# Performance work log

Hardware: AMD Instinct MI355X
Metric: run time of the kernel (lower is better)

The kernel has to match this reference:

```python
import jax, jax.numpy as jnp
from jax import lax
import numpy as np

B, T, D = 8192, 187, 1
H, C = 128, 5


def setup_inputs() -> dict:
    key = jax.random.key(0)
    k1, k2, k3, k4 = jax.random.split(key, 4)
    x = jax.random.normal(k1, (B, T, D), dtype=jnp.float32)
    # SimpleRNN params: kernel W [D,H], recurrent kernel U [H,H] (orthogonal-ish), bias b [H]
    W = jax.random.normal(k2, (D, H), dtype=jnp.float32) * (1.0 / np.sqrt(D))
    U = jax.random.normal(k3, (H, H), dtype=jnp.float32) * (1.0 / np.sqrt(H))
    b = jnp.zeros((H,), dtype=jnp.float32)
    # Dense head params
    Wd = jax.random.normal(k4, (H, C), dtype=jnp.float32) * (1.0 / np.sqrt(H))
    bd = jnp.zeros((C,), dtype=jnp.float32)
    return {"x": x, "W": W, "U": U, "b": b, "Wd": Wd, "bd": bd}


def reference(x, W, U, b, Wd, bd):
    # SimpleRNN (tanh) recurrence over time, returning final hidden state only
    # (return_sequences=False, dropout inactive at inference).
    h0 = jnp.zeros((x.shape[0], U.shape[0]), dtype=x.dtype)
    xt_seq = jnp.swapaxes(x, 0, 1)  # [T, B, D]

    def step(h, xt):
        h_new = jnp.tanh(xt @ W + h @ U + b)
        return h_new, None

    hT, _ = lax.scan(step, h0, xt_seq)
    # Dense softmax classifier head
    logits = hT @ Wd + bd  # [B, C]
    return jax.nn.softmax(logits, axis=-1)
```

## Files before the change

### kernel.cpp

```cpp
#include <hip/hip_runtime.h>
#include <hip/hip_bf16.h>


#define BT 8192
#define TS 187
#define HD 128
#define NC 5

typedef float    f32x4  __attribute__((ext_vector_type(4)));
typedef _Float16 f16x8  __attribute__((ext_vector_type(8)));
typedef __fp16   fp16x2 __attribute__((ext_vector_type(2)));
typedef unsigned int u32;
typedef u32      u32x2  __attribute__((ext_vector_type(2)));

__device__ __forceinline__ float tanh_fast(float v) {
    float e = __expf(2.0f * v);
    float r = __builtin_amdgcn_rcpf(e + 1.0f);
    return fmaf(-2.0f, r, 1.0f);
}

__device__ __forceinline__ u32 pk16(float a, float b) {
    fp16x2 p = __builtin_amdgcn_cvt_pkrtz(a, b);
    return __builtin_bit_cast(u32, p);
}

union frag_u { f16x8 v; u32 w[4]; };

__device__ __forceinline__ void pin_frag(f16x8& f) {
    frag_u pu; pu.v = f;
    asm volatile("" : "+v"(pu.w[0]), "+v"(pu.w[1]), "+v"(pu.w[2]), "+v"(pu.w[3]));
    f = pu.v;
}

__global__ __launch_bounds__(512, 4)
void rnn_fused(const float* __restrict__ xg, const float* __restrict__ wg,
               const float* __restrict__ ug, const float* __restrict__ bg,
               const float* __restrict__ wdg, const float* __restrict__ bdg,
               float* __restrict__ outg)
{
    __shared__ u32   xb[2][4][64][4];
    __shared__ float xs[TS][16];
    __shared__ float lg[8][16][NC];

    const int tid  = threadIdx.x;
    const int w    = tid >> 6;
    const int lane = tid & 63;
    const int l15  = lane & 15;
    const int l4   = lane >> 4;
    const int b0   = blockIdx.x * 16;
    const int Tw   = w >> 1;
    const int hw   = w & 1;

    #pragma unroll
    for (int r = 0; r < 6; ++r) {
        const int idx = r * 512 + tid;
        const int bb  = idx / 192;
        const int ss  = idx % 192;
        if (ss < TS)
            xs[ss][bb] = xg[(long)(b0 + bb) * TS + ss];
    }

    f16x8 uf0, uf1, uf2, uf3;
    {
        const int j = 16*w + l15;
        #pragma unroll
        for (int e = 0; e < 8; ++e) {
            const int i = 16*(e>>2) + 4*l4 + (e&3);
            uf0[e] = (_Float16)ug[(i      )*HD + j];
            uf1[e] = (_Float16)ug[(i + 32 )*HD + j];
            uf2[e] = (_Float16)ug[(i + 64 )*HD + j];
            uf3[e] = (_Float16)ug[(i + 96 )*HD + j];
        }
    }
    pin_frag(uf0); pin_frag(uf1); pin_frag(uf2); pin_frag(uf3);

    float wv[4], bv[4];
    #pragma unroll
    for (int q = 0; q < 4; ++q) {
        const int j = 16*w + 4*l4 + q;
        wv[q] = wg[j];
        bv[q] = bg[j];
    }

    f16x8 h0 = (f16x8)(_Float16)0.0f;
    f16x8 h1 = h0, h2 = h0, h3 = h0;

    __syncthreads();
    float xv = xs[0][l15];

    f32x4 acc;

#define STEP(BUF, SN)                                                       \
    {                                                                       \
        const float xnext = xs[(SN)][l15];                                  \
        f32x4 a0, a1;                                                       \
        _Pragma("unroll") for (int q = 0; q < 4; ++q) {                     \
            a0[q] = fmaf(xv, wv[q], bv[q]); a1[q] = 0.0f;                   \
        }                                                                   \
        a0 = __builtin_amdgcn_mfma_f32_16x16x32_f16(uf0, h0, a0, 0, 0, 0);  \
        a1 = __builtin_amdgcn_mfma_f32_16x16x32_f16(uf2, h2, a1, 0, 0, 0);  \
        a0 = __builtin_amdgcn_mfma_f32_16x16x32_f16(uf1, h1, a0, 0, 0, 0);  \
        a1 = __builtin_amdgcn_mfma_f32_16x16x32_f16(uf3, h3, a1, 0, 0, 0);  \
        _Pragma("unroll") for (int q = 0; q < 4; ++q)                       \
            acc[q] = tanh_fast(a0[q] + a1[q]);                              \
        u32x2 pk;                                                           \
        pk[0] = pk16(acc[0], acc[1]);                                       \
        pk[1] = pk16(acc[2], acc[3]);                                       \
        *(u32x2*)&xb[(BUF)][Tw][lane][2*hw] = pk;                           \
        __syncthreads();                                                    \
        h0 = *(const f16x8*)&xb[(BUF)][0][lane][0];                         \
        h1 = *(const f16x8*)&xb[(BUF)][1][lane][0];                         \
        h2 = *(const f16x8*)&xb[(BUF)][2][lane][0];                         \
        h3 = *(const f16x8*)&xb[(BUF)][3][lane][0];                         \
        xv = xnext;                                                         \
    }

    for (int k = 0; k < 93; ++k) {
        STEP(0, 2*k + 1);
        STEP(1, 2*k + 2);
    }
    STEP(0, TS - 1);
#undef STEP

    float p[NC];
    #pragma unroll
    for (int c = 0; c < NC; ++c) p[c] = 0.0f;
    #pragma unroll
    for (int q = 0; q < 4; ++q) {
        const int j = 16*w + 4*l4 + q;
        #pragma unroll
        for (int c = 0; c < NC; ++c)
            p[c] = fmaf(acc[q], wdg[j*NC + c], p[c]);
    }
    #pragma unroll
    for (int c = 0; c < NC; ++c) {
        p[c] += __shfl_xor(p[c], 16, 64);
        p[c] += __shfl_xor(p[c], 32, 64);
    }
    if (l4 == 0) {
        #pragma unroll
        for (int c = 0; c < NC; ++c) lg[w][l15][c] = p[c];
    }
    __syncthreads();

    if (tid < 16) {
        float l[NC];
        #pragma unroll
        for (int c = 0; c < NC; ++c) {
            l[c] = bdg[c];
            #pragma unroll
            for (int ww = 0; ww < 8; ++ww) l[c] += lg[ww][tid][c];
        }
        float m = l[0];
        #pragma unroll
        for (int c = 1; c < NC; ++c) m = fmaxf(m, l[c]);
        float e[NC], ssum = 0.0f;
        #pragma unroll
        for (int c = 0; c < NC; ++c) { e[c] = __expf(l[c] - m); ssum += e[c]; }
        const float rs = 1.0f / ssum;
        #pragma unroll
        for (int c = 0; c < NC; ++c)
            outg[(long)(b0 + tid)*NC + c] = e[c] * rs;
    }
}

extern "C" void kernel_launch(void* const* d_in, const int* in_sizes, int n_in,
                              void* d_out, int out_size, void* d_ws, size_t ws_size,
                              hipStream_t stream) {
    const float* x  = (const float*)d_in[0];
    const float* W  = (const float*)d_in[1];
    const float* U  = (const float*)d_in[2];
    const float* b  = (const float*)d_in[3];
    const float* Wd = (const float*)d_in[4];
    const float* bd = (const float*)d_in[5];
    float* out = (float*)d_out;

    rnn_fused<<<BT / 16, 512, 0, stream>>>(x, W, U, b, Wd, bd, out);
}
```

Before: 85.42 us.

## Process two batch tiles per block and fold tanh scaling into weights

Each block now handles 32 batch rows as two independent 16-row tiles. Their MFMA chains and tanh computations interleave, so the latency of one tile's dependent recurrence can be hidden behind the other's, and there is one barrier per step for both tiles. The 2*log2(e) factor is folded into U, W and b at load time, so tanh uses a raw exp2 and the bias enters as the MFMA accumulator init. The trade-off is half as many blocks (256), more registers and LDS per block, and a lowered occupancy hint, which may leave CUs underused on a 256-CU part.

```diff
diff --git a/kernel.cpp b/kernel.cpp
--- a/kernel.cpp
+++ b/kernel.cpp
@@ -13,8 +13,18 @@
 typedef unsigned int u32;
 typedef u32      u32x2  __attribute__((ext_vector_type(2)));
 
-__device__ __forceinline__ float tanh_fast(float v) {
-    float e = __expf(2.0f * v);
+#define PRE 2.885390081777927f
+
+__device__ __forceinline__ float exp2_fast(float v) {
+#if __has_builtin(__builtin_amdgcn_exp2f)
+    return __builtin_amdgcn_exp2f(v);
+#else
+    return exp2f(v);
+#endif
+}
+
+__device__ __forceinline__ float tanh_pre(float vp) {
+    float e = exp2_fast(vp);
     float r = __builtin_amdgcn_rcpf(e + 1.0f);
     return fmaf(-2.0f, r, 1.0f);
 }
@@ -32,32 +42,34 @@
     f = pu.v;
 }
 
-__global__ __launch_bounds__(512, 4)
+__global__ __launch_bounds__(512, 2)
 void rnn_fused(const float* __restrict__ xg, const float* __restrict__ wg,
                const float* __restrict__ ug, const float* __restrict__ bg,
                const float* __restrict__ wdg, const float* __restrict__ bdg,
                float* __restrict__ outg)
 {
-    __shared__ u32   xb[2][4][64][4];
-    __shared__ float xs[TS][16];
-    __shared__ float lg[8][16][NC];
+    __shared__ u32   xbA[2][4][64][4];
+    __shared__ u32   xbB[2][4][64][4];
+    __shared__ float xs2[2][TS][16];
+    __shared__ float lgA[8][16][NC];
+    __shared__ float lgB[8][16][NC];
 
     const int tid  = threadIdx.x;
     const int w    = tid >> 6;
     const int lane = tid & 63;
     const int l15  = lane & 15;
     const int l4   = lane >> 4;
-    const int b0   = blockIdx.x * 16;
+    const int b0   = blockIdx.x * 32;
     const int Tw   = w >> 1;
     const int hw   = w & 1;
 
     #pragma unroll
-    for (int r = 0; r < 6; ++r) {
+    for (int r = 0; r < 12; ++r) {
         const int idx = r * 512 + tid;
         const int bb  = idx / 192;
         const int ss  = idx % 192;
         if (ss < TS)
-            xs[ss][bb] = xg[(long)(b0 + bb) * TS + ss];
+            xs2[bb >> 4][ss][bb & 15] = xg[(long)(b0 + bb) * TS + ss];
     }
 
     f16x8 uf0, uf1, uf2, uf3;
@@ -66,53 +78,67 @@
         #pragma unroll
         for (int e = 0; e < 8; ++e) {
             const int i = 16*(e>>2) + 4*l4 + (e&3);
-            uf0[e] = (_Float16)ug[(i      )*HD + j];
-            uf1[e] = (_Float16)ug[(i + 32 )*HD + j];
-            uf2[e] = (_Float16)ug[(i + 64 )*HD + j];
-            uf3[e] = (_Float16)ug[(i + 96 )*HD + j];
+            uf0[e] = (_Float16)(PRE * ug[(i      )*HD + j]);
+            uf1[e] = (_Float16)(PRE * ug[(i + 32 )*HD + j]);
+            uf2[e] = (_Float16)(PRE * ug[(i + 64 )*HD + j]);
+            uf3[e] = (_Float16)(PRE * ug[(i + 96 )*HD + j]);
         }
     }
     pin_frag(uf0); pin_frag(uf1); pin_frag(uf2); pin_frag(uf3);
 
-    float wv[4], bv[4];
+    float wv[4]; f32x4 bvv;
     #pragma unroll
     for (int q = 0; q < 4; ++q) {
         const int j = 16*w + 4*l4 + q;
-        wv[q] = wg[j];
-        bv[q] = bg[j];
-    }
-
-    f16x8 h0 = (f16x8)(_Float16)0.0f;
-    f16x8 h1 = h0, h2 = h0, h3 = h0;
+        wv[q]  = PRE * wg[j];
+        bvv[q] = PRE * bg[j];
+    }
+
+    f16x8 hA0 = (f16x8)(_Float16)0.0f;
+    f16x8 hA1 = hA0, hA2 = hA0, hA3 = hA0;
+    f16x8 hB0 = hA0, hB1 = hA0, hB2 = hA0, hB3 = hA0;
 
     __syncthreads();
-    float xv = xs[0][l15];
-
-    f32x4 acc;
-
-#define STEP(BUF, SN)                                                       \
-    {                                                                       \
-        const float xnext = xs[(SN)][l15];                                  \
-        f32x4 a0, a1;                                                       \
-        _Pragma("unroll") for (int q = 0; q < 4; ++q) {                     \
-            a0[q] = fmaf(xv, wv[q], bv[q]); a1[q] = 0.0f;                   \
-        }                                                                   \
-        a0 = __builtin_amdgcn_mfma_f32_16x16x32_f16(uf0, h0, a0, 0, 0, 0);  \
-        a1 = __builtin_amdgcn_mfma_f32_16x16x32_f16(uf2, h2, a1, 0, 0, 0);  \
-        a0 = __builtin_amdgcn_mfma_f32_16x16x32_f16(uf1, h1, a0, 0, 0, 0);  \
-        a1 = __builtin_amdgcn_mfma_f32_16x16x32_f16(uf3, h3, a1, 0, 0, 0);  \
-        _Pragma("unroll") for (int q = 0; q < 4; ++q)                       \
-            acc[q] = tanh_fast(a0[q] + a1[q]);                              \
-        u32x2 pk;                                                           \
-        pk[0] = pk16(acc[0], acc[1]);                                       \
-        pk[1] = pk16(acc[2], acc[3]);                                       \
-        *(u32x2*)&xb[(BUF)][Tw][lane][2*hw] = pk;                           \
-        __syncthreads();                                                    \
-        h0 = *(const f16x8*)&xb[(BUF)][0][lane][0];                         \
-        h1 = *(const f16x8*)&xb[(BUF)][1][lane][0];                         \
-        h2 = *(const f16x8*)&xb[(BUF)][2][lane][0];                         \
-        h3 = *(const f16x8*)&xb[(BUF)][3][lane][0];                         \
-        xv = xnext;                                                         \
+    float xvA = xs2[0][0][l15];
+    float xvB = xs2[1][0][l15];
+
+    f32x4 accA, accB;
+
+#define STEP(BUF, SN)                                                        \
+    {                                                                        \
+        const float xAn = xs2[0][(SN)][l15];                                 \
+        const float xBn = xs2[1][(SN)][l15];                                 \
+        f32x4 a0, a1, c0, c1;                                                \
+        _Pragma("unroll") for (int q = 0; q < 4; ++q) {                      \
+            a0[q] = xvA * wv[q]; c0[q] = xvB * wv[q];                        \
+        }                                                                    \
+        a0 = __builtin_amdgcn_mfma_f32_16x16x32_f16(uf0, hA0, a0,  0, 0, 0); \
+        c0 = __builtin_amdgcn_mfma_f32_16x16x32_f16(uf0, hB0, c0,  0, 0, 0); \
+        a1 = __builtin_amdgcn_mfma_f32_16x16x32_f16(uf2, hA2, bvv, 0, 0, 0); \
+        c1 = __builtin_amdgcn_mfma_f32_16x16x32_f16(uf2, hB2, bvv, 0, 0, 0); \
+        a0 = __builtin_amdgcn_mfma_f32_16x16x32_f16(uf1, hA1, a0,  0, 0, 0); \
+        c0 = __builtin_amdgcn_mfma_f32_16x16x32_f16(uf1, hB1, c0,  0, 0, 0); \
+        a1 = __builtin_amdgcn_mfma_f32_16x16x32_f16(uf3, hA3, a1,  0, 0, 0); \
+        c1 = __builtin_amdgcn_mfma_f32_16x16x32_f16(uf3, hB3, c1,  0, 0, 0); \
+        _Pragma("unroll") for (int q = 0; q < 4; ++q) {                      \
+            accA[q] = tanh_pre(a0[q] + a1[q]);                               \
+            accB[q] = tanh_pre(c0[q] + c1[q]);                               \
+        }                                                                    \
+        u32x2 pA, pB;                                                        \
+        pA[0] = pk16(accA[0], accA[1]); pA[1] = pk16(accA[2], accA[3]);      \
+        pB[0] = pk16(accB[0], accB[1]); pB[1] = pk16(accB[2], accB[3]);      \
+        *(u32x2*)&xbA[(BUF)][Tw][lane][2*hw] = pA;                           \
+        *(u32x2*)&xbB[(BUF)][Tw][lane][2*hw] = pB;                           \
+        __syncthreads();                                                     \
+        hA0 = *(const f16x8*)&xbA[(BUF)][0][lane][0];                        \
+        hA1 = *(const f16x8*)&xbA[(BUF)][1][lane][0];                        \
+        hA2 = *(const f16x8*)&xbA[(BUF)][2][lane][0];                        \
+        hA3 = *(const f16x8*)&xbA[(BUF)][3][lane][0];                        \
+        hB0 = *(const f16x8*)&xbB[(BUF)][0][lane][0];                        \
+        hB1 = *(const f16x8*)&xbB[(BUF)][1][lane][0];                        \
+        hB2 = *(const f16x8*)&xbB[(BUF)][2][lane][0];                        \
+        hB3 = *(const f16x8*)&xbB[(BUF)][3][lane][0];                        \
+        xvA = xAn; xvB = xBn;                                                \
     }
 
     for (int k = 0; k < 93; ++k) {
@@ -122,34 +148,41 @@
     STEP(0, TS - 1);
 #undef STEP
 
-    float p[NC];
-    #pragma unroll
-    for (int c = 0; c < NC; ++c) p[c] = 0.0f;
+    float pA[NC], pB[NC];
+    #pragma unroll
+    for (int c = 0; c < NC; ++c) { pA[c] = 0.0f; pB[c] = 0.0f; }
     #pragma unroll
     for (int q = 0; q < 4; ++q) {
         const int j = 16*w + 4*l4 + q;
         #pragma unroll
-        for (int c = 0; c < NC; ++c)
-            p[c] = fmaf(acc[q], wdg[j*NC + c], p[c]);
+        for (int c = 0; c < NC; ++c) {
+            const float wd = wdg[j*NC + c];
+            pA[c] = fmaf(accA[q], wd, pA[c]);
+            pB[c] = fmaf(accB[q], wd, pB[c]);
+        }
     }
     #pragma unroll
     for (int c = 0; c < NC; ++c) {
-        p[c] += __shfl_xor(p[c], 16, 64);
-        p[c] += __shfl_xor(p[c], 32, 64);
+        pA[c] += __shfl_xor(pA[c], 16, 64);
+        pA[c] += __shfl_xor(pA[c], 32, 64);
+        pB[c] += __shfl_xor(pB[c], 16, 64);
+        pB[c] += __shfl_xor(pB[c], 32, 64);
     }
     if (l4 == 0) {
         #pragma unroll
-        for (int c = 0; c < NC; ++c) lg[w][l15][c] = p[c];
+        for (int c = 0; c < NC; ++c) { lgA[w][l15][c] = pA[c]; lgB[w][l15][c] = pB[c]; }
     }
     __syncthreads();
 
-    if (tid < 16) {
+    if (tid < 32) {
+        const int tile = tid >> 4, bi = tid & 15;
         float l[NC];
         #pragma unroll
         for (int c = 0; c < NC; ++c) {
             l[c] = bdg[c];
             #pragma unroll
-            for (int ww = 0; ww < 8; ++ww) l[c] += lg[ww][tid][c];
+            for (int ww = 0; ww < 8; ++ww)
+                l[c] += tile ? lgB[ww][bi][c] : lgA[ww][bi][c];
         }
         float m = l[0];
         #pragma unroll
@@ -160,7 +193,7 @@
         const float rs = 1.0f / ssum;
         #pragma unroll
         for (int c = 0; c < NC; ++c)
-            outg[(long)(b0 + tid)*NC + c] = e[c] * rs;
+            outg[(long)(b0 + tile*16 + bi)*NC + c] = e[c] * rs;
     }
 }
 
@@ -175,5 +208,5 @@
     const float* bd = (const float*)d_in[5];
     float* out = (float*)d_out;
 
-    rnn_fused<<<BT / 16, 512, 0, stream>>>(x, W, U, b, Wd, bd, out);
-}
+    rnn_fused<<<BT / 32, 512, 0, stream>>>(x, W, U, b, Wd, bd, out);
+}
```

Result: slower. 91.52 us (+7.1%).

## Halve waves per block, give each wave two output tiles, prescale tanh constant

Applied to the files above, without the earlier changes.

Each block now uses 4 waves instead of 8, and each wave computes two 16-column slices of the hidden state (8 MFMAs per step instead of 4). The recurrent weights, input weights and bias are prescaled by 2/ln2 so tanh can use a raw exp2 without an extra multiply. The bias now seeds one accumulator directly, removing an FMA. Each wave writes a full 16-byte fragment per step, and the per-step barrier spans fewer waves. The trade-off is more serial MFMA work and more registers per wave, with less wave-level parallelism per block.

```diff
diff --git a/kernel.cpp b/kernel.cpp
--- a/kernel.cpp
+++ b/kernel.cpp
@@ -11,10 +11,20 @@
 typedef _Float16 f16x8  __attribute__((ext_vector_type(8)));
 typedef __fp16   fp16x2 __attribute__((ext_vector_type(2)));
 typedef unsigned int u32;
-typedef u32      u32x2  __attribute__((ext_vector_type(2)));
+typedef u32      u32x4  __attribute__((ext_vector_type(4)));
 
-__device__ __forceinline__ float tanh_fast(float v) {
-    float e = __expf(2.0f * v);
+#define PRE 2.885390081777927f
+
+__device__ __forceinline__ float exp2_fast(float v) {
+#if __has_builtin(__builtin_amdgcn_exp2f)
+    return __builtin_amdgcn_exp2f(v);
+#else
+    return exp2f(v);
+#endif
+}
+
+__device__ __forceinline__ float tanh_pre(float vp) {
+    float e = exp2_fast(vp);
     float r = __builtin_amdgcn_rcpf(e + 1.0f);
     return fmaf(-2.0f, r, 1.0f);
 }
@@ -32,7 +42,7 @@
     f = pu.v;
 }
 
-__global__ __launch_bounds__(512, 4)
+__global__ __launch_bounds__(256, 4)
 void rnn_fused(const float* __restrict__ xg, const float* __restrict__ wg,
                const float* __restrict__ ug, const float* __restrict__ bg,
                const float* __restrict__ wdg, const float* __restrict__ bdg,
@@ -40,7 +50,7 @@
 {
     __shared__ u32   xb[2][4][64][4];
     __shared__ float xs[TS][16];
-    __shared__ float lg[8][16][NC];
+    __shared__ float lg[4][16][NC];
 
     const int tid  = threadIdx.x;
     const int w    = tid >> 6;
@@ -48,38 +58,42 @@
     const int l15  = lane & 15;
     const int l4   = lane >> 4;
     const int b0   = blockIdx.x * 16;
-    const int Tw   = w >> 1;
-    const int hw   = w & 1;
 
     #pragma unroll
-    for (int r = 0; r < 6; ++r) {
-        const int idx = r * 512 + tid;
+    for (int r = 0; r < 12; ++r) {
+        const int idx = r * 256 + tid;
         const int bb  = idx / 192;
         const int ss  = idx % 192;
         if (ss < TS)
             xs[ss][bb] = xg[(long)(b0 + bb) * TS + ss];
     }
 
-    f16x8 uf0, uf1, uf2, uf3;
+    f16x8 uf00, uf01, uf02, uf03;
+    f16x8 uf10, uf11, uf12, uf13;
     {
-        const int j = 16*w + l15;
+        const int j0 = 32*w + l15;
         #pragma unroll
         for (int e = 0; e < 8; ++e) {
             const int i = 16*(e>>2) + 4*l4 + (e&3);
-            uf0[e] = (_Float16)ug[(i      )*HD + j];
-            uf1[e] = (_Float16)ug[(i + 32 )*HD + j];
-            uf2[e] = (_Float16)ug[(i + 64 )*HD + j];
-            uf3[e] = (_Float16)ug[(i + 96 )*HD + j];
+            uf00[e] = (_Float16)(PRE * ug[(i     )*HD + j0]);
+            uf01[e] = (_Float16)(PRE * ug[(i + 32)*HD + j0]);
+            uf02[e] = (_Float16)(PRE * ug[(i + 64)*HD + j0]);
+            uf03[e] = (_Float16)(PRE * ug[(i + 96)*HD + j0]);
+            uf10[e] = (_Float16)(PRE * ug[(i     )*HD + j0 + 16]);
+            uf11[e] = (_Float16)(PRE * ug[(i + 32)*HD + j0 + 16]);
+            uf12[e] = (_Float16)(PRE * ug[(i + 64)*HD + j0 + 16]);
+            uf13[e] = (_Float16)(PRE * ug[(i + 96)*HD + j0 + 16]);
         }
     }
-    pin_frag(uf0); pin_frag(uf1); pin_frag(uf2); pin_frag(uf3);
+    pin_frag(uf00); pin_frag(uf01); pin_frag(uf02); pin_frag(uf03);
+    pin_frag(uf10); pin_frag(uf11); pin_frag(uf12); pin_frag(uf13);
 
-    float wv[4], bv[4];
+    float wv0[4], wv1[4]; f32x4 bv0, bv1;
     #pragma unroll
     for (int q = 0; q < 4; ++q) {
-        const int j = 16*w + 4*l4 + q;
-        wv[q] = wg[j];
-        bv[q] = bg[j];
+        const int j = 32*w + 4*l4 + q;
+        wv0[q] = PRE * wg[j];      bv0[q] = PRE * bg[j];
+        wv1[q] = PRE * wg[j + 16]; bv1[q] = PRE * bg[j + 16];
     }
 
     f16x8 h0 = (f16x8)(_Float16)0.0f;
@@ -88,31 +102,37 @@
     __syncthreads();
     float xv = xs[0][l15];
 
-    f32x4 acc;
+    f32x4 accA, accB;
 
-#define STEP(BUF, SN)                                                       \
-    {                                                                       \
-        const float xnext = xs[(SN)][l15];                                  \
-        f32x4 a0, a1;                                                       \
-        _Pragma("unroll") for (int q = 0; q < 4; ++q) {                     \
-            a0[q] = fmaf(xv, wv[q], bv[q]); a1[q] = 0.0f;                   \
-        }                                                                   \
-        a0 = __builtin_amdgcn_mfma_f32_16x16x32_f16(uf0, h0, a0, 0, 0, 0);  \
-        a1 = __builtin_amdgcn_mfma_f32_16x16x32_f16(uf2, h2, a1, 0, 0, 0);  \
-        a0 = __builtin_amdgcn_mfma_f32_16x16x32_f16(uf1, h1, a0, 0, 0, 0);  \
-        a1 = __builtin_amdgcn_mfma_f32_16x16x32_f16(uf3, h3, a1, 0, 0, 0);  \
-        _Pragma("unroll") for (int q = 0; q < 4; ++q)                       \
-            acc[q] = tanh_fast(a0[q] + a1[q]);                              \
-        u32x2 pk;                                                           \
-        pk[0] = pk16(acc[0], acc[1]);                                       \
-        pk[1] = pk16(acc[2], acc[3]);                                       \
-        *(u32x2*)&xb[(BUF)][Tw][lane][2*hw] = pk;                           \
-        __syncthreads();                                                    \
-        h0 = *(const f16x8*)&xb[(BUF)][0][lane][0];                         \
-        h1 = *(const f16x8*)&xb[(BUF)][1][lane][0];                         \
-        h2 = *(const f16x8*)&xb[(BUF)][2][lane][0];                         \
-        h3 = *(const f16x8*)&xb[(BUF)][3][lane][0];                         \
-        xv = xnext;                                                         \
+#define STEP(BUF, SN)                                                         \
+    {                                                                         \
+        const float xnext = xs[(SN)][l15];                                    \
+        f32x4 a0, a1, b0c, b1c;                                               \
+        _Pragma("unroll") for (int q = 0; q < 4; ++q) {                       \
+            a0[q] = xv * wv0[q]; b0c[q] = xv * wv1[q];                        \
+        }                                                                     \
+        a0  = __builtin_amdgcn_mfma_f32_16x16x32_f16(uf00, h0, a0,  0, 0, 0); \
+        b0c = __builtin_amdgcn_mfma_f32_16x16x32_f16(uf10, h0, b0c, 0, 0, 0); \
+        a1  = __builtin_amdgcn_mfma_f32_16x16x32_f16(uf02, h2, bv0, 0, 0, 0); \
+        b1c = __builtin_amdgcn_mfma_f32_16x16x32_f16(uf12, h2, bv1, 0, 0, 0); \
+        a0  = __builtin_amdgcn_mfma_f32_16x16x32_f16(uf01, h1, a0,  0, 0, 0); \
+        b0c = __builtin_amdgcn_mfma_f32_16x16x32_f16(uf11, h1, b0c, 0, 0, 0); \
+        a1  = __builtin_amdgcn_mfma_f32_16x16x32_f16(uf03, h3, a1,  0, 0, 0); \
+        b1c = __builtin_amdgcn_mfma_f32_16x16x32_f16(uf13, h3, b1c, 0, 0, 0); \
+        _Pragma("unroll") for (int q = 0; q < 4; ++q) {                       \
+            accA[q] = tanh_pre(a0[q] + a1[q]);                                \
+            accB[q] = tanh_pre(b0c[q] + b1c[q]);                              \
+        }                                                                     \
+        u32x4 F;                                                              \
+        F[0] = pk16(accA[0], accA[1]); F[1] = pk16(accA[2], accA[3]);         \
+        F[2] = pk16(accB[0], accB[1]); F[3] = pk16(accB[2], accB[3]);         \
+        *(u32x4*)&xb[(BUF)][w][lane][0] = F;                                  \
+        __syncthreads();                                                      \
+        h0 = *(const f16x8*)&xb[(BUF)][0][lane][0];                           \
+        h1 = *(const f16x8*)&xb[(BUF)][1][lane][0];                           \
+        h2 = *(const f16x8*)&xb[(BUF)][2][lane][0];                           \
+        h3 = *(const f16x8*)&xb[(BUF)][3][lane][0];                           \
+        xv = xnext;                                                           \
     }
 
     for (int k = 0; k < 93; ++k) {
@@ -127,10 +147,12 @@
     for (int c = 0; c < NC; ++c) p[c] = 0.0f;
     #pragma unroll
     for (int q = 0; q < 4; ++q) {
-        const int j = 16*w + 4*l4 + q;
+        const int j = 32*w + 4*l4 + q;
         #pragma unroll
-        for (int c = 0; c < NC; ++c)
-            p[c] = fmaf(acc[q], wdg[j*NC + c], p[c]);
+        for (int c = 0; c < NC; ++c) {
+            p[c] = fmaf(accA[q], wdg[j*NC + c], p[c]);
+            p[c] = fmaf(accB[q], wdg[(j+16)*NC + c], p[c]);
+        }
     }
     #pragma unroll
     for (int c = 0; c < NC; ++c) {
@@ -146,11 +168,8 @@
     if (tid < 16) {
         float l[NC];
         #pragma unroll
-        for (int c = 0; c < NC; ++c) {
-            l[c] = bdg[c];
-            #pragma unroll
-            for (int ww = 0; ww < 8; ++ww) l[c] += lg[ww][tid][c];
-        }
+        for (int c = 0; c < NC; ++c)
+            l[c] = bdg[c] + lg[0][tid][c] + lg[1][tid][c] + lg[2][tid][c] + lg[3][tid][c];
         float m = l[0];
         #pragma unroll
         for (int c = 1; c < NC; ++c) m = fmaxf(m, l[c]);
@@ -175,5 +194,5 @@
     const float* bd = (const float*)d_in[5];
     float* out = (float*)d_out;
 
-    rnn_fused<<<BT / 16, 512, 0, stream>>>(x, W, U, b, Wd, bd, out);
+    rnn_fused<<<BT / 16, 256, 0, stream>>>(x, W, U, b, Wd, bd, out);
 }
```

After: 89.09 us. 1.04x slower.
